# Optimization experiments

Hardware: AMD Instinct MI355X
Metric: run time of the kernel (lower is better)

## Reference

```python
import jax, jax.numpy as jnp
import numpy as np

OUT_FEATURES = 4096
IN_FEATURES = 4096
RANK = 64
ALPHA = 1.0
SCALING = ALPHA / float(RANK)  # w1 direct, w2 factored -> effective_alpha = alpha


def setup_inputs() -> dict:
    key = jax.random.key(0)
    k_x, k_w1, k_a, k_b = jax.random.split(key, 4)
    x = jax.random.normal(k_x, (4, 2048, IN_FEATURES), dtype=jnp.float32)
    lokr_w1 = jax.random.normal(k_w1, (8, 8), dtype=jnp.float32)        # [out_l, in_m]
    lokr_w2_a = jax.random.normal(k_a, (512, RANK), dtype=jnp.float32)  # [out_k, rank]
    lokr_w2_b = jax.random.normal(k_b, (RANK, 512), dtype=jnp.float32)  # [rank, in_n]
    return {"x": x, "lokr_w1": lokr_w1, "lokr_w2_a": lokr_w2_a, "lokr_w2_b": lokr_w2_b}


def reference(x, lokr_w1, lokr_w2_a, lokr_w2_b):
    # w2 = w2_a @ w2_b : [out_k, in_n]
    w2 = lokr_w2_a @ lokr_w2_b
    # kron(w1, w2): element (i*out_k + k, j*in_n + l) = w1[i,j] * w2[k,l]
    out_l, in_m = lokr_w1.shape
    out_k, in_n = w2.shape
    diff = jnp.einsum('ij,kl->ikjl', lokr_w1, w2).reshape(out_l * out_k, in_m * in_n)
    diff = diff * SCALING  # [out_features, in_features]
    # F.linear(x, diff) = x @ diff.T
    return jnp.einsum('bsi,oi->bso', x, diff)
```

## Files before the change

### kernel.cpp

```cpp
#include <hip/hip_runtime.h>
#include <hip/hip_bf16.h>


typedef __attribute__((ext_vector_type(4))) float f32x4;
typedef __attribute__((ext_vector_type(8))) short s16x8;

__device__ inline unsigned short f2bf(float f) {
    unsigned u = __float_as_uint(f);
    u += 0x7FFF + ((u >> 16) & 1);
    return (unsigned short)(u >> 16);
}

__global__ void lokr_pre(const float* __restrict__ w1,
                         const float* __restrict__ a,
                         const float* __restrict__ b,
                         unsigned short* __restrict__ b_bf,
                         unsigned short* __restrict__ a_bf,
                         float* __restrict__ w1s) {
    int i = blockIdx.x * 256 + threadIdx.x;
    if (i < 32768) {
        b_bf[i] = f2bf(b[i]);
        a_bf[i] = f2bf(a[i]);
    }
    if (i < 64) w1s[i] = w1[i] * (1.0f / 64.0f);
}

__global__ __launch_bounds__(256) void lokr_main(
    const float* __restrict__ x,
    const unsigned short* __restrict__ b_bf,
    const unsigned short* __restrict__ a_bf,
    const float* __restrict__ w1s,
    float* __restrict__ out)
{
    __shared__ float w1_s[64];
    __shared__ __attribute__((aligned(16))) unsigned short v_lds[4][16 * 72];

    const int tid = threadIdx.x;
    if (tid < 64) w1_s[tid] = w1s[tid];
    __syncthreads();

    const int wave = tid >> 6;
    const int lane = tid & 63;
    const int col  = lane & 15;
    const int quad = lane >> 4;

    const long p0 = ((long)blockIdx.x * 4 + wave) * 2;

    f32x4 acc0 = {0.f,0.f,0.f,0.f}, acc1 = acc0, acc2 = acc0, acc3 = acc0;
    const float* xrow = x + (p0 * 8 + col) * 512 + quad * 8;
    const unsigned short* bbase = b_bf + col * 512 + quad * 8;

    #pragma unroll 4
    for (int ks = 0; ks < 16; ++ks) {
        const float* ap = xrow + ks * 32;
        float4 lo = *(const float4*)(ap);
        float4 hi = *(const float4*)(ap + 4);
        s16x8 af;
        af[0] = (short)f2bf(lo.x); af[1] = (short)f2bf(lo.y);
        af[2] = (short)f2bf(lo.z); af[3] = (short)f2bf(lo.w);
        af[4] = (short)f2bf(hi.x); af[5] = (short)f2bf(hi.y);
        af[6] = (short)f2bf(hi.z); af[7] = (short)f2bf(hi.w);
        const unsigned short* bp = bbase + ks * 32;
        s16x8 bf0 = *(const s16x8*)(bp);
        s16x8 bf1 = *(const s16x8*)(bp + 16 * 512);
        s16x8 bf2 = *(const s16x8*)(bp + 32 * 512);
        s16x8 bf3 = *(const s16x8*)(bp + 48 * 512);
        acc0 = __builtin_amdgcn_mfma_f32_16x16x32_bf16(af, bf0, acc0, 0, 0, 0);
        acc1 = __builtin_amdgcn_mfma_f32_16x16x32_bf16(af, bf1, acc1, 0, 0, 0);
        acc2 = __builtin_amdgcn_mfma_f32_16x16x32_bf16(af, bf2, acc2, 0, 0, 0);
        acc3 = __builtin_amdgcn_mfma_f32_16x16x32_bf16(af, bf3, acc3, 0, 0, 0);
    }

    {
        const int lp = quad >> 1;
        const int oi_base = (quad & 1) * 4;
        f32x4 accs[4] = {acc0, acc1, acc2, acc3};
        #pragma unroll
        for (int rt = 0; rt < 4; ++rt) {
            float own[4], oth[4], tij[8];
            own[0] = accs[rt][0]; own[1] = accs[rt][1];
            own[2] = accs[rt][2]; own[3] = accs[rt][3];
            #pragma unroll
            for (int j = 0; j < 4; ++j) oth[j] = __shfl_xor(own[j], 16);
            if ((quad & 1) == 0) {
                #pragma unroll
                for (int j = 0; j < 4; ++j) { tij[j] = own[j]; tij[4 + j] = oth[j]; }
            } else {
                #pragma unroll
                for (int j = 0; j < 4; ++j) { tij[j] = oth[j]; tij[4 + j] = own[j]; }
            }
            #pragma unroll
            for (int oo = 0; oo < 4; ++oo) {
                const int oi = oi_base + oo;
                float v = 0.f;
                #pragma unroll
                for (int j = 0; j < 8; ++j) v += w1_s[oi * 8 + j] * tij[j];
                v_lds[wave][(lp * 8 + oi) * 72 + rt * 16 + col] = f2bf(v);
            }
        }
    }
    __syncthreads();

    const unsigned short* vbase = &v_lds[wave][col * 72 + quad * 8];
    s16x8 va0 = *(const s16x8*)(vbase);
    s16x8 va1 = *(const s16x8*)(vbase + 32);

    const unsigned short* abase = a_bf + col * 64 + quad * 8;
    float* outp = out + p0 * 4096;

    #pragma unroll 4
    for (int nt = 0; nt < 32; ++nt) {
        const unsigned short* apn = abase + nt * (16 * 64);
        s16x8 vb0 = *(const s16x8*)(apn);
        s16x8 vb1 = *(const s16x8*)(apn + 32);
        f32x4 c = {0.f, 0.f, 0.f, 0.f};
        c = __builtin_amdgcn_mfma_f32_16x16x32_bf16(va0, vb0, c, 0, 0, 0);
        c = __builtin_amdgcn_mfma_f32_16x16x32_bf16(va1, vb1, c, 0, 0, 0);
        #pragma unroll
        for (int reg = 0; reg < 4; ++reg) {
            const int row = quad * 4 + reg;
            outp[(long)(row >> 3) * 4096 + (row & 7) * 512 + nt * 16 + col] = c[reg];
        }
    }
}

extern "C" void kernel_launch(void* const* d_in, const int* in_sizes, int n_in,
                              void* d_out, int out_size, void* d_ws, size_t ws_size,
                              hipStream_t stream) {
    const float* x  = (const float*)d_in[0];
    const float* w1 = (const float*)d_in[1];
    const float* a  = (const float*)d_in[2];
    const float* b  = (const float*)d_in[3];

    unsigned short* b_bf = (unsigned short*)d_ws;
    unsigned short* a_bf = b_bf + 32768;
    float*          w1s  = (float*)(a_bf + 32768);

    lokr_pre<<<128, 256, 0, stream>>>(w1, a, b, b_bf, a_bf, w1s);
    lokr_main<<<1024, 256, 0, stream>>>(x, b_bf, a_bf, w1s, (float*)d_out);
}
```

Baseline: 269.1 us.

## Split each row-pair's work across two waves and prefetch next k-step loads

Each pair of waves now shares one 16-row tile. Each wave computes half of the rank dimension in the first GEMM and half of the output columns in the second. The grid doubles to 2048 blocks and the launch bounds request 8 blocks per CU, which raises parallelism and cuts per-wave register use. The k-loop is now fully unrolled and software-pipelined, so the next x and B loads are issued before the current MFMAs. In exchange, every x row is loaded twice (once by each wave of the pair), which raises global read traffic on what is a bandwidth-heavy input.

```diff
diff --git a/kernel.cpp b/kernel.cpp
--- a/kernel.cpp
+++ b/kernel.cpp
@@ -25,7 +25,7 @@
     if (i < 64) w1s[i] = w1[i] * (1.0f / 64.0f);
 }
 
-__global__ __launch_bounds__(256) void lokr_main(
+__global__ __launch_bounds__(256, 8) void lokr_main(
     const float* __restrict__ x,
     const unsigned short* __restrict__ b_bf,
     const unsigned short* __restrict__ a_bf,
@@ -33,7 +33,7 @@
     float* __restrict__ out)
 {
     __shared__ float w1_s[64];
-    __shared__ __attribute__((aligned(16))) unsigned short v_lds[4][16 * 72];
+    __shared__ __attribute__((aligned(16))) unsigned short v_lds[2][16 * 72];
 
     const int tid = threadIdx.x;
     if (tid < 64) w1_s[tid] = w1s[tid];
@@ -43,40 +43,49 @@
     const int lane = tid & 63;
     const int col  = lane & 15;
     const int quad = lane >> 4;
+    const int pair = wave >> 1;
+    const int rh   = wave & 1;
 
-    const long p0 = ((long)blockIdx.x * 4 + wave) * 2;
+    const long gp = ((long)blockIdx.x * 2 + pair) * 2;
 
-    f32x4 acc0 = {0.f,0.f,0.f,0.f}, acc1 = acc0, acc2 = acc0, acc3 = acc0;
-    const float* xrow = x + (p0 * 8 + col) * 512 + quad * 8;
-    const unsigned short* bbase = b_bf + col * 512 + quad * 8;
+    f32x4 acc0 = {0.f,0.f,0.f,0.f}, acc1 = acc0;
+    const float* xrow = x + (gp * 8 + col) * 512 + quad * 8;
+    const unsigned short* bbase = b_bf + (rh * 32 + col) * 512 + quad * 8;
 
-    #pragma unroll 4
+    float4 lo = *(const float4*)(xrow);
+    float4 hi = *(const float4*)(xrow + 4);
+    s16x8 bf0 = *(const s16x8*)(bbase);
+    s16x8 bf1 = *(const s16x8*)(bbase + 16 * 512);
+
+    #pragma unroll
     for (int ks = 0; ks < 16; ++ks) {
-        const float* ap = xrow + ks * 32;
-        float4 lo = *(const float4*)(ap);
-        float4 hi = *(const float4*)(ap + 4);
+        float4 nlo, nhi; s16x8 nb0, nb1;
+        if (ks < 15) {
+            const float* ap = xrow + (ks + 1) * 32;
+            nlo = *(const float4*)(ap);
+            nhi = *(const float4*)(ap + 4);
+            const unsigned short* bp = bbase + (ks + 1) * 32;
+            nb0 = *(const s16x8*)(bp);
+            nb1 = *(const s16x8*)(bp + 16 * 512);
+        } else {
+            nlo = lo; nhi = hi; nb0 = bf0; nb1 = bf1;
+        }
         s16x8 af;
         af[0] = (short)f2bf(lo.x); af[1] = (short)f2bf(lo.y);
         af[2] = (short)f2bf(lo.z); af[3] = (short)f2bf(lo.w);
         af[4] = (short)f2bf(hi.x); af[5] = (short)f2bf(hi.y);
         af[6] = (short)f2bf(hi.z); af[7] = (short)f2bf(hi.w);
-        const unsigned short* bp = bbase + ks * 32;
-        s16x8 bf0 = *(const s16x8*)(bp);
-        s16x8 bf1 = *(const s16x8*)(bp + 16 * 512);
-        s16x8 bf2 = *(const s16x8*)(bp + 32 * 512);
-        s16x8 bf3 = *(const s16x8*)(bp + 48 * 512);
         acc0 = __builtin_amdgcn_mfma_f32_16x16x32_bf16(af, bf0, acc0, 0, 0, 0);
         acc1 = __builtin_amdgcn_mfma_f32_16x16x32_bf16(af, bf1, acc1, 0, 0, 0);
-        acc2 = __builtin_amdgcn_mfma_f32_16x16x32_bf16(af, bf2, acc2, 0, 0, 0);
-        acc3 = __builtin_amdgcn_mfma_f32_16x16x32_bf16(af, bf3, acc3, 0, 0, 0);
+        lo = nlo; hi = nhi; bf0 = nb0; bf1 = nb1;
     }
 
     {
         const int lp = quad >> 1;
         const int oi_base = (quad & 1) * 4;
-        f32x4 accs[4] = {acc0, acc1, acc2, acc3};
+        f32x4 accs[2] = {acc0, acc1};
         #pragma unroll
-        for (int rt = 0; rt < 4; ++rt) {
+        for (int rt = 0; rt < 2; ++rt) {
             float own[4], oth[4], tij[8];
             own[0] = accs[rt][0]; own[1] = accs[rt][1];
             own[2] = accs[rt][2]; own[3] = accs[rt][3];
@@ -95,21 +104,22 @@
                 float v = 0.f;
                 #pragma unroll
                 for (int j = 0; j < 8; ++j) v += w1_s[oi * 8 + j] * tij[j];
-                v_lds[wave][(lp * 8 + oi) * 72 + rt * 16 + col] = f2bf(v);
+                v_lds[pair][(lp * 8 + oi) * 72 + rh * 32 + rt * 16 + col] = f2bf(v);
             }
         }
     }
     __syncthreads();
 
-    const unsigned short* vbase = &v_lds[wave][col * 72 + quad * 8];
+    const unsigned short* vbase = &v_lds[pair][col * 72 + quad * 8];
     s16x8 va0 = *(const s16x8*)(vbase);
     s16x8 va1 = *(const s16x8*)(vbase + 32);
 
     const unsigned short* abase = a_bf + col * 64 + quad * 8;
-    float* outp = out + p0 * 4096;
+    float* outp = out + gp * 4096;
 
     #pragma unroll 4
-    for (int nt = 0; nt < 32; ++nt) {
+    for (int t = 0; t < 16; ++t) {
+        const int nt = rh * 16 + t;
         const unsigned short* apn = abase + nt * (16 * 64);
         s16x8 vb0 = *(const s16x8*)(apn);
         s16x8 vb1 = *(const s16x8*)(apn + 32);
@@ -137,5 +147,5 @@
     float*          w1s  = (float*)(a_bf + 32768);
 
     lokr_pre<<<128, 256, 0, stream>>>(w1, a, b, b_bf, a_bf, w1s);
-    lokr_main<<<1024, 256, 0, stream>>>(x, b_bf, a_bf, w1s, (float*)d_out);
+    lokr_main<<<2048, 256, 0, stream>>>(x, b_bf, a_bf, w1s, (float*)d_out);
 }
```

Measured after the change: 286.7 us. 1.07x slower.

## Stage x tiles in LDS with double buffering and enlarge per-block row tile

Applied to the files above, without the earlier changes.

Each block now handles 128 rows of the reshaped x. It converts x to bf16 into a double-buffered LDS tile so that all four waves share it, and prefetches the next k-slice into registers while the MFMAs run. Each wave covers 16 rank columns across 8 row tiles instead of a private 16-row strip, which cuts redundant b loads, and output writes become 16-column chunks per wave. The cost is more LDS, more register pressure (launch_bounds 256,4) and a barrier per k-step, with half as many blocks in the grid.

```diff
diff --git a/kernel.cpp b/kernel.cpp
--- a/kernel.cpp
+++ b/kernel.cpp
@@ -4,6 +4,7 @@
 
 typedef __attribute__((ext_vector_type(4))) float f32x4;
 typedef __attribute__((ext_vector_type(8))) short s16x8;
+typedef __attribute__((ext_vector_type(4))) short s16x4;
 
 __device__ inline unsigned short f2bf(float f) {
     unsigned u = __float_as_uint(f);
@@ -25,101 +26,133 @@
     if (i < 64) w1s[i] = w1[i] * (1.0f / 64.0f);
 }
 
-__global__ __launch_bounds__(256) void lokr_main(
+#define LSTR 72
+
+__global__ __launch_bounds__(256, 4) void lokr_main(
     const float* __restrict__ x,
     const unsigned short* __restrict__ b_bf,
     const unsigned short* __restrict__ a_bf,
     const float* __restrict__ w1s,
     float* __restrict__ out)
 {
+    __shared__ __attribute__((aligned(16))) unsigned short xs[2][128 * LSTR];
+    __shared__ __attribute__((aligned(16))) unsigned short vs[128 * LSTR];
     __shared__ float w1_s[64];
-    __shared__ __attribute__((aligned(16))) unsigned short v_lds[4][16 * 72];
 
-    const int tid = threadIdx.x;
-    if (tid < 64) w1_s[tid] = w1s[tid];
+    const int t    = threadIdx.x;
+    const int wave = t >> 6;
+    const int lane = t & 63;
+    const int col  = lane & 15;
+    const int quad = lane >> 4;
+    const long rowbase = (long)blockIdx.x * 128;
+
+    if (t < 64) w1_s[t] = w1s[t];
+
+    const int lrow = t >> 4;
+    const int lcol = (t & 15) * 4;
+
+    float4 xb[8];
+    {
+        const float* xg = x + (rowbase + lrow) * 512 + lcol;
+        #pragma unroll
+        for (int i = 0; i < 8; ++i)
+            xb[i] = *(const float4*)(xg + (long)i * 16 * 512);
+    }
+    #pragma unroll
+    for (int i = 0; i < 8; ++i) {
+        s16x4 h;
+        h[0] = (short)f2bf(xb[i].x); h[1] = (short)f2bf(xb[i].y);
+        h[2] = (short)f2bf(xb[i].z); h[3] = (short)f2bf(xb[i].w);
+        *(s16x4*)&xs[0][(lrow + i * 16) * LSTR + lcol] = h;
+    }
     __syncthreads();
 
-    const int wave = tid >> 6;
-    const int lane = tid & 63;
-    const int col  = lane & 15;
-    const int quad = lane >> 4;
+    f32x4 acc[8];
+    #pragma unroll
+    for (int m = 0; m < 8; ++m) acc[m] = (f32x4){0.f, 0.f, 0.f, 0.f};
 
-    const long p0 = ((long)blockIdx.x * 4 + wave) * 2;
+    const unsigned short* brow = b_bf + (wave * 16 + col) * 512 + quad * 8;
 
-    f32x4 acc0 = {0.f,0.f,0.f,0.f}, acc1 = acc0, acc2 = acc0, acc3 = acc0;
-    const float* xrow = x + (p0 * 8 + col) * 512 + quad * 8;
-    const unsigned short* bbase = b_bf + col * 512 + quad * 8;
-
-    #pragma unroll 4
-    for (int ks = 0; ks < 16; ++ks) {
-        const float* ap = xrow + ks * 32;
-        float4 lo = *(const float4*)(ap);
-        float4 hi = *(const float4*)(ap + 4);
-        s16x8 af;
-        af[0] = (short)f2bf(lo.x); af[1] = (short)f2bf(lo.y);
-        af[2] = (short)f2bf(lo.z); af[3] = (short)f2bf(lo.w);
-        af[4] = (short)f2bf(hi.x); af[5] = (short)f2bf(hi.y);
-        af[6] = (short)f2bf(hi.z); af[7] = (short)f2bf(hi.w);
-        const unsigned short* bp = bbase + ks * 32;
-        s16x8 bf0 = *(const s16x8*)(bp);
-        s16x8 bf1 = *(const s16x8*)(bp + 16 * 512);
-        s16x8 bf2 = *(const s16x8*)(bp + 32 * 512);
-        s16x8 bf3 = *(const s16x8*)(bp + 48 * 512);
-        acc0 = __builtin_amdgcn_mfma_f32_16x16x32_bf16(af, bf0, acc0, 0, 0, 0);
-        acc1 = __builtin_amdgcn_mfma_f32_16x16x32_bf16(af, bf1, acc1, 0, 0, 0);
-        acc2 = __builtin_amdgcn_mfma_f32_16x16x32_bf16(af, bf2, acc2, 0, 0, 0);
-        acc3 = __builtin_amdgcn_mfma_f32_16x16x32_bf16(af, bf3, acc3, 0, 0, 0);
+    #pragma unroll 2
+    for (int s = 0; s < 8; ++s) {
+        s16x8 bf0 = *(const s16x8*)(brow + s * 64);
+        s16x8 bf1 = *(const s16x8*)(brow + s * 64 + 32);
+        if (s < 7) {
+            const float* xg = x + (rowbase + lrow) * 512 + (s + 1) * 64 + lcol;
+            #pragma unroll
+            for (int i = 0; i < 8; ++i)
+                xb[i] = *(const float4*)(xg + (long)i * 16 * 512);
+        }
+        const unsigned short* xa = &xs[s & 1][col * LSTR + quad * 8];
+        #pragma unroll
+        for (int m = 0; m < 8; ++m) {
+            s16x8 a0 = *(const s16x8*)(xa + m * 16 * LSTR);
+            s16x8 a1 = *(const s16x8*)(xa + m * 16 * LSTR + 32);
+            acc[m] = __builtin_amdgcn_mfma_f32_16x16x32_bf16(a0, bf0, acc[m], 0, 0, 0);
+            acc[m] = __builtin_amdgcn_mfma_f32_16x16x32_bf16(a1, bf1, acc[m], 0, 0, 0);
+        }
+        if (s < 7) {
+            #pragma unroll
+            for (int i = 0; i < 8; ++i) {
+                s16x4 h;
+                h[0] = (short)f2bf(xb[i].x); h[1] = (short)f2bf(xb[i].y);
+                h[2] = (short)f2bf(xb[i].z); h[3] = (short)f2bf(xb[i].w);
+                *(s16x4*)&xs[(s + 1) & 1][(lrow + i * 16) * LSTR + lcol] = h;
+            }
+        }
+        __syncthreads();
     }
 
-    {
-        const int lp = quad >> 1;
-        const int oi_base = (quad & 1) * 4;
-        f32x4 accs[4] = {acc0, acc1, acc2, acc3};
+    #pragma unroll
+    for (int m = 0; m < 8; ++m) {
+        float own[4], oth[4], tij[8];
         #pragma unroll
-        for (int rt = 0; rt < 4; ++rt) {
-            float own[4], oth[4], tij[8];
-            own[0] = accs[rt][0]; own[1] = accs[rt][1];
-            own[2] = accs[rt][2]; own[3] = accs[rt][3];
+        for (int j = 0; j < 4; ++j) own[j] = acc[m][j];
+        #pragma unroll
+        for (int j = 0; j < 4; ++j) oth[j] = __shfl_xor(own[j], 16);
+        if ((quad & 1) == 0) {
             #pragma unroll
-            for (int j = 0; j < 4; ++j) oth[j] = __shfl_xor(own[j], 16);
-            if ((quad & 1) == 0) {
-                #pragma unroll
-                for (int j = 0; j < 4; ++j) { tij[j] = own[j]; tij[4 + j] = oth[j]; }
-            } else {
-                #pragma unroll
-                for (int j = 0; j < 4; ++j) { tij[j] = oth[j]; tij[4 + j] = own[j]; }
-            }
+            for (int j = 0; j < 4; ++j) { tij[j] = own[j]; tij[4 + j] = oth[j]; }
+        } else {
             #pragma unroll
-            for (int oo = 0; oo < 4; ++oo) {
-                const int oi = oi_base + oo;
-                float v = 0.f;
-                #pragma unroll
-                for (int j = 0; j < 8; ++j) v += w1_s[oi * 8 + j] * tij[j];
-                v_lds[wave][(lp * 8 + oi) * 72 + rt * 16 + col] = f2bf(v);
-            }
+            for (int j = 0; j < 4; ++j) { tij[j] = oth[j]; tij[4 + j] = own[j]; }
+        }
+        const int plocal = m * 2 + (quad >> 1);
+        const int oib = (quad & 1) * 4;
+        #pragma unroll
+        for (int oo = 0; oo < 4; ++oo) {
+            float v = 0.f;
+            #pragma unroll
+            for (int j = 0; j < 8; ++j) v += w1_s[(oib + oo) * 8 + j] * tij[j];
+            vs[(plocal * 8 + oib + oo) * LSTR + wave * 16 + col] = f2bf(v);
         }
     }
     __syncthreads();
 
-    const unsigned short* vbase = &v_lds[wave][col * 72 + quad * 8];
-    s16x8 va0 = *(const s16x8*)(vbase);
-    s16x8 va1 = *(const s16x8*)(vbase + 32);
+    s16x8 va0[8], va1[8];
+    #pragma unroll
+    for (int m = 0; m < 8; ++m) {
+        const unsigned short* vp = &vs[(m * 16 + col) * LSTR + quad * 8];
+        va0[m] = *(const s16x8*)(vp);
+        va1[m] = *(const s16x8*)(vp + 32);
+    }
 
-    const unsigned short* abase = a_bf + col * 64 + quad * 8;
-    float* outp = out + p0 * 4096;
+    const unsigned short* ab = a_bf + (wave * 128 + col) * 64 + quad * 8;
+    float* ob = out + (long)blockIdx.x * 65536 + wave * 128 + col;
 
-    #pragma unroll 4
-    for (int nt = 0; nt < 32; ++nt) {
-        const unsigned short* apn = abase + nt * (16 * 64);
-        s16x8 vb0 = *(const s16x8*)(apn);
-        s16x8 vb1 = *(const s16x8*)(apn + 32);
-        f32x4 c = {0.f, 0.f, 0.f, 0.f};
-        c = __builtin_amdgcn_mfma_f32_16x16x32_bf16(va0, vb0, c, 0, 0, 0);
-        c = __builtin_amdgcn_mfma_f32_16x16x32_bf16(va1, vb1, c, 0, 0, 0);
+    for (int nt = 0; nt < 8; ++nt) {
+        s16x8 af0 = *(const s16x8*)(ab + nt * 16 * 64);
+        s16x8 af1 = *(const s16x8*)(ab + nt * 16 * 64 + 32);
         #pragma unroll
-        for (int reg = 0; reg < 4; ++reg) {
-            const int row = quad * 4 + reg;
-            outp[(long)(row >> 3) * 4096 + (row & 7) * 512 + nt * 16 + col] = c[reg];
+        for (int m = 0; m < 8; ++m) {
+            f32x4 c = {0.f, 0.f, 0.f, 0.f};
+            c = __builtin_amdgcn_mfma_f32_16x16x32_bf16(va0[m], af0, c, 0, 0, 0);
+            c = __builtin_amdgcn_mfma_f32_16x16x32_bf16(va1[m], af1, c, 0, 0, 0);
+            #pragma unroll
+            for (int reg = 0; reg < 4; ++reg) {
+                const int rl = m * 16 + quad * 4 + reg;
+                ob[(long)rl * 512 + nt * 16] = c[reg];
+            }
         }
     }
 }
@@ -137,5 +170,5 @@
     float*          w1s  = (float*)(a_bf + 32768);
 
     lokr_pre<<<128, 256, 0, stream>>>(w1, a, b, b_bf, a_bf, w1s);
-    lokr_main<<<1024, 256, 0, stream>>>(x, b_bf, a_bf, w1s, (float*)d_out);
+    lokr_main<<<512, 256, 0, stream>>>(x, b_bf, a_bf, w1s, (float*)d_out);
 }
```

Measured after the change: 268.1 us. About the same (-0.4%).
